# Performance work log

Measured on AMD Instinct MI355X. Metric: run time of the kernel, lower is better.

## Reference

```python
import jax, jax.numpy as jnp
import numpy as np

C = 64
RED = 4            # attention reduction: conv_match C -> C//RED
CR = C // RED      # 16, also MultiScaleSpatialAttention reduced channels
N_HASHES = 4
CHUNK = 512
RES_SCALE = 0.1
EPS = 5e-5


def conv2d(x, w, b=None, padding=0, groups=1):
    out = jax.lax.conv_general_dilated(
        x, w, (1, 1), [(padding, padding), (padding, padding)],
        dimension_numbers=('NCHW', 'OIHW', 'NCHW'), feature_group_count=groups)
    if b is not None:
        out = out + b[None, :, None, None]
    return out


def ds_conv(x, pw_w, dw_w, dw_b, padding):
    # pointwise (no bias) then depthwise (bias)
    x = conv2d(x, pw_w)
    return conv2d(x, dw_w, dw_b, padding=padding, groups=dw_w.shape[0])


def pool2(x, mode):
    B, Cc, H, W = x.shape
    xr = x.reshape(B, Cc, H // 2, 2, W // 2, 2)
    return xr.max(axis=(3, 5)) if mode == 'max' else xr.mean(axis=(3, 5))


def bilinear_ac(x, out_h, out_w):
    # bilinear interpolation with align_corners=True (matches F.interpolate)
    B, Cc, h, w = x.shape
    def coords(n_in, n_out):
        pos = jnp.arange(n_out, dtype=x.dtype) * ((n_in - 1) / (n_out - 1))
        lo = jnp.floor(pos).astype(jnp.int32)
        hi = jnp.minimum(lo + 1, n_in - 1)
        frac = pos - lo.astype(x.dtype)
        return lo, hi, frac
    lo_h, hi_h, fh = coords(h, out_h)
    x = x[:, :, lo_h, :] * (1 - fh)[None, None, :, None] + x[:, :, hi_h, :] * fh[None, None, :, None]
    lo_w, hi_w, fw = coords(w, out_w)
    x = x[:, :, :, lo_w] * (1 - fw) + x[:, :, :, hi_w] * fw
    return x


def sparse_attn(x, wm, bm, wa, ba, rot):
    # NLSN-style LSH-chunked non-local sparse attention
    N, Cc, H, W = x.shape
    L = H * W
    xe = conv2d(x, wm, bm).reshape(N, -1, L).transpose(0, 2, 1)   # [N,L,Ce]
    ye = conv2d(x, wa, ba).reshape(N, -1, L).transpose(0, 2, 1)   # [N,L,C]
    Ce = xe.shape[-1]
    n_chunks = L // CHUNK                     # L multiple of CHUNK here -> no padding
    buckets = min(n_chunks + n_chunks % 2, 128)
    # LSH hashing (rot: [Ce, n_hashes, buckets//2])
    rv = jnp.einsum('blf,fhi->bhli', xe, rot)
    rv = jnp.concatenate([rv, -rv], axis=-1)  # [N,nh,L,buckets]
    codes = jnp.argmax(rv, axis=-1) + (jnp.arange(N_HASHES) * buckets)[None, :, None]
    codes = codes.reshape(N, -1)              # [N, nh*L]
    idx = jnp.argsort(codes, axis=-1)
    undo = jnp.argsort(idx, axis=-1)
    mod_idx = idx % L
    xs = jnp.take_along_axis(xe, mod_idx[:, :, None], axis=1)     # [N,nh*L,Ce]
    ys = jnp.take_along_axis(ye, mod_idx[:, :, None], axis=1)     # [N,nh*L,C]
    xb = xs.reshape(N, N_HASHES, n_chunks, CHUNK, Ce)
    yb = ys.reshape(N, N_HASHES, n_chunks, CHUNK, Cc)
    xm = xb / jnp.maximum(jnp.linalg.norm(xb, axis=-1, keepdims=True), EPS)
    def adj(t):  # add previous / next bucket (circular)
        return jnp.concatenate([t, jnp.roll(t, 1, axis=2), jnp.roll(t, -1, axis=2)], axis=3)
    xm3, yb3 = adj(xm), adj(yb)
    raw = jnp.einsum('bhkie,bhkje->bhkij', xb, xm3)               # [N,nh,k,CHUNK,3*CHUNK]
    bscore = jax.nn.logsumexp(raw, axis=-1, keepdims=True)
    score = jnp.exp(raw - bscore)
    ret = jnp.einsum('bhkij,bhkje->bhkie', score, yb3)            # [N,nh,k,CHUNK,C]
    ret = ret.reshape(N, N_HASHES * L, Cc)
    bscore = bscore.reshape(N, N_HASHES * L)
    ret = jnp.take_along_axis(ret, undo[:, :, None], axis=1).reshape(N, N_HASHES, L, Cc)
    bscore = jnp.take_along_axis(bscore, undo, axis=1).reshape(N, N_HASHES, L, 1)
    probs = jax.nn.softmax(bscore, axis=1)                        # over hash rounds
    out = (ret * probs).sum(axis=1)                               # [N,L,C]
    out = out.transpose(0, 2, 1).reshape(N, Cc, H, W)
    return out * RES_SCALE + x


def setup_inputs() -> dict:
    key = jax.random.key(0)
    ks = iter(jax.random.split(key, 40))
    w = lambda *s: jax.random.normal(next(ks), s, jnp.float32) * 0.1
    inp = {
        'x': jax.random.normal(next(ks), (2, C, 128, 128), jnp.float32),
        'spa_down_w': w(CR, C, 1, 1), 'spa_down_b': w(CR),
        's0_pw_w': w(2 * CR, CR, 1, 1), 's0_dw_w': w(2 * CR, 1, 1, 1), 's0_dw_b': w(2 * CR),
        'br3_pw_w': w(CR, CR, 1, 1), 'br3_dw_w': w(CR, 1, 3, 3), 'br3_dw_b': w(CR),
        'br5_pw_w': w(CR, CR, 1, 1), 'br5_dw_w': w(CR, 1, 5, 5), 'br5_dw_b': w(CR),
        'br7_pw_w': w(CR, CR, 1, 1), 'br7_dw_w': w(CR, 1, 7, 7), 'br7_dw_b': w(CR),
        'fusion_w': w(C, 8 * CR, 1, 1), 'fusion_b': w(C),
        'resid_w': w(C, C, 1, 1), 'resid_b': w(C),
        'ca_w1': w(C // 16, C, 1, 1), 'ca_b1': w(C // 16),
        'ca_w2': w(C, C // 16, 1, 1), 'ca_b2': w(C),
        'conv1x1_w': w(C, C, 1, 1), 'conv1x1_b': w(C),
        'match_w': w(CR, C, 1, 1), 'match_b': w(CR),
        'asm_w': w(C, C, 1, 1), 'asm_b': w(C),
        'rot': jax.random.normal(next(ks), (CR, N_HASHES, 16), jnp.float32),  # buckets//2 = 16
        'collect_w': w(C, C, 1, 1), 'collect_b': w(C),
    }
    return inp


def reference(x, spa_down_w, spa_down_b, s0_pw_w, s0_dw_w, s0_dw_b,
              br3_pw_w, br3_dw_w, br3_dw_b, br5_pw_w, br5_dw_w, br5_dw_b,
              br7_pw_w, br7_dw_w, br7_dw_b, fusion_w, fusion_b,
              resid_w, resid_b, ca_w1, ca_b1, ca_w2, ca_b2,
              conv1x1_w, conv1x1_b, match_w, match_b, asm_w, asm_b, rot,
              collect_w, collect_b):
    B, Cc, H, W = x.shape
    # --- MultiScaleSpatialAttention ---
    xr = conv2d(x, spa_down_w, spa_down_b)                # [B,16,H,W]
    s0 = ds_conv(xr, s0_pw_w, s0_dw_w, s0_dw_b, padding=0)
    feats = [s0]
    for pw, dw, db, pad in ((br3_pw_w, br3_dw_w, br3_dw_b, 1),
                            (br5_pw_w, br5_dw_w, br5_dw_b, 2),
                            (br7_pw_w, br7_dw_w, br7_dw_b, 3)):
        mx = ds_conv(pool2(xr, 'max'), pw, dw, db, pad)
        av = ds_conv(pool2(xr, 'avg'), pw, dw, db, pad)
        feats.append(jnp.concatenate([bilinear_ac(mx, H, W), bilinear_ac(av, H, W)], axis=1))
    attn = jax.nn.sigmoid(conv2d(jnp.concatenate(feats, axis=1), fusion_w, fusion_b))
    spa_mask = x * attn + conv2d(x, resid_w, resid_b)
    # --- CALayer ---
    y = x.mean(axis=(2, 3), keepdims=True)
    y = jax.nn.sigmoid(conv2d(jax.nn.relu(conv2d(y, ca_w1, ca_b1)), ca_w2, ca_b2))
    spe_mask = x * y
    # --- combine + SparseMaskConv (n_layers=1: attention then 1x1 collect) ---
    mask = conv2d(spa_mask + spe_mask, conv1x1_w, conv1x1_b) + x
    fea = sparse_attn(mask, match_w, match_b, asm_w, asm_b, rot)
    out1 = conv2d(fea, collect_w, collect_b)
    return out1 + x
```

## Files before the change

### kernel.cpp

```cpp
#include <hip/hip_runtime.h>
#include <math.h>

static constexpr int NB = 2;
static constexpr int NC = 64;
static constexpr int NHp = 128, NWp = 128;
static constexpr int NL = NHp * NWp;
static constexpr int NCR = 16;
static constexpr int NL2 = 64 * 64;
static constexpr int NHASH = 4;
static constexpr int CHUNKSZ = 512;
static constexpr int NCHUNKS = 32;
static constexpr int TOT = NHASH * NL;
static constexpr int NKEY = 128;
static constexpr int NTILE = 256;
static constexpr int TILESZ = TOT / NTILE;

typedef _Float16 half4 __attribute__((ext_vector_type(4)));
typedef _Float16 half8 __attribute__((ext_vector_type(8)));
typedef float f32x4 __attribute__((ext_vector_type(4)));

#if __has_builtin(__builtin_amdgcn_exp2f)
  #define EXP2F(x) __builtin_amdgcn_exp2f(x)
#else
  #define EXP2F(x) __expf(0.69314718f*(x))
#endif

static constexpr size_t OFF_MASK = 0;
static constexpr size_t OFF_FEA  = OFF_MASK + (size_t)NB*NC*NL;
static constexpr size_t OFF_XE   = OFF_FEA  + (size_t)NB*NC*NL;
static constexpr size_t OFF_XEH  = OFF_XE   + (size_t)NB*NL*NCR;
static constexpr size_t OFF_XENH = OFF_XEH  + (size_t)NB*NL*NCR/2;
static constexpr size_t OFF_VS   = OFF_XENH + (size_t)NB*NL*NCR/2;
static constexpr size_t OFF_RET  = OFF_VS   + (size_t)NB*TOT*NC/2;
static constexpr size_t OFF_BSC  = OFF_RET  + (size_t)NB*TOT*NC/2;
static constexpr size_t OFF_INT  = OFF_BSC  + (size_t)NB*TOT;
static constexpr size_t IOFF_CODES = 0;
static constexpr size_t IOFF_IDX   = IOFF_CODES + (size_t)NB*TOT;
static constexpr size_t IOFF_UNDO  = IOFF_IDX   + (size_t)NB*TOT;
static constexpr size_t IOFF_HIST  = IOFF_UNDO  + (size_t)NB*TOT;
static constexpr size_t IOFF_OFFS  = IOFF_HIST  + (size_t)NB*NKEY*NTILE/2;
static constexpr size_t IOFF_END   = IOFF_OFFS  + (size_t)NB*NKEY*NTILE/2;
static constexpr size_t OFF_CAY = OFF_INT + IOFF_END;
static constexpr size_t OFF_CAS = OFF_CAY + 128;
static constexpr size_t OFF_CRW = OFF_CAS + 128;
static constexpr size_t OFF_CRB = OFF_CRW + 4096;
static constexpr size_t OFF_QS = OFF_FEA;
static constexpr size_t OFF_KS = OFF_QS + (size_t)NB*TOT*NCR/2;
static_assert(OFF_KS + (size_t)NB*TOT*NCR/2 <= OFF_XE, "qs/ks fit in fea region");
static constexpr size_t OFF_PTMP  = OFF_FEA;
static constexpr size_t OFF_DWT   = OFF_PTMP + (size_t)6*NB*NCR*NL2;
static_assert(OFF_DWT + (size_t)6*NB*NCR*NL2 <= OFF_XE, "halfres overlay fits");
static constexpr size_t OFF_XR    = OFF_XE;
static constexpr size_t OFF_FEATS = OFF_XR + (size_t)NB*NCR*NL;
static_assert(OFF_FEATS + (size_t)NB*128*NL <= OFF_RET, "feats overlay fits");
static constexpr size_t OFF_PRE1  = OFF_FEA;

__device__ __forceinline__ float sigmoidf_(float v){ return 1.0f/(1.0f + expf(-v)); }


__global__ __launch_bounds__(256,4) void k_xr(const float* __restrict__ x,
                     const float* __restrict__ w,
                     const float* __restrict__ b, float* __restrict__ xr){
  int gid = blockIdx.x*256 + threadIdx.x;
  int pix = gid >> 1, hf = gid & 1;
  int bb = pix >> 14, p = pix & (NL-1);
  const float* xi = x + (size_t)bb*NC*NL + (size_t)hf*32*NL + p;
  float acc[16];
  #pragma unroll
  for (int oc=0; oc<16; ++oc) acc[oc] = hf ? 0.f : b[oc];
  for (int ic0=0; ic0<32; ic0+=16){
    float r[16];
    #pragma unroll
    for (int j=0; j<16; ++j) r[j] = xi[(size_t)(ic0+j)*NL];
    #pragma unroll
    for (int oc=0; oc<16; ++oc){
      #pragma unroll
      for (int j=0; j<16; ++j) acc[oc] += r[j]*w[oc*64 + hf*32 + ic0 + j];
    }
  }
  #pragma unroll
  for (int oc=0; oc<16; ++oc) acc[oc] += __shfl_xor(acc[oc], 1, 64);
  if (!hf){
    float* xo = xr + (size_t)bb*NCR*NL + p;
    #pragma unroll
    for (int oc=0; oc<16; ++oc) xo[(size_t)oc*NL] = acc[oc];
  }
}

__global__ __launch_bounds__(256,4) void k_s0(const float* __restrict__ xr,
                     const float* __restrict__ pw,
                     const float* __restrict__ dww, const float* __restrict__ dwb,
                     float* __restrict__ feats){
  int gid = blockIdx.x*256 + threadIdx.x;
  int oc0 = blockIdx.y*16;
  int bb = gid >> 14, p = gid & (NL-1);
  const float* xi = xr + (size_t)bb*NCR*NL + p;
  float r[16];
  #pragma unroll
  for (int ic=0; ic<16; ++ic) r[ic] = xi[(size_t)ic*NL];
  float* fo = feats + (size_t)bb*128*NL + p;
  #pragma unroll
  for (int j=0; j<16; ++j){
    int oc = oc0 + j;
    float s = 0.f;
    #pragma unroll
    for (int ic=0; ic<16; ++ic) s += r[ic]*pw[oc*16+ic];
    fo[(size_t)oc*NL] = s*dww[oc] + dwb[oc];
  }
}

__global__ void k_pw16_all(const float* __restrict__ xr,
                           const float* __restrict__ w0, const float* __restrict__ w1,
                           const float* __restrict__ w2, float* __restrict__ out){
  int gid = blockIdx.x*256 + threadIdx.x;
  if (gid >= 6*NB*NL2) return;
  int p = gid & (NL2-1); int t = gid >> 12; int bb = t & 1; int combo = t >> 1;
  int br = combo >> 1, mode = combo & 1;
  const float* w = (br==0) ? w0 : (br==1) ? w1 : w2;
  int y = p >> 6, x2 = p & 63;
  float r[16];
  #pragma unroll
  for (int ic=0; ic<16; ++ic){
    const float* base = xr + (size_t)(bb*NCR + ic)*NL + (size_t)(2*y)*NWp + 2*x2;
    float a = base[0], b_ = base[1], c_ = base[NWp], d = base[NWp+1];
    r[ic] = mode ? 0.25f*(a+b_+c_+d) : fmaxf(fmaxf(a,b_), fmaxf(c_,d));
  }
  float* oo = out + ((size_t)(combo*NB + bb)*NCR)*NL2 + p;
  #pragma unroll
  for (int oc=0; oc<16; ++oc){
    float s = 0.f;
    #pragma unroll
    for (int ic=0; ic<16; ++ic) s += r[ic]*w[oc*16+ic];
    oo[(size_t)oc*NL2] = s;
  }
}

__global__ void k_dw_all(const float* __restrict__ in,
                         const float* __restrict__ w3, const float* __restrict__ b3,
                         const float* __restrict__ w5, const float* __restrict__ b5,
                         const float* __restrict__ w7, const float* __restrict__ b7,
                         float* __restrict__ out){
  int gid = blockIdx.x*256 + threadIdx.x;
  if (gid >= 6*NB*NCR*NL2) return;
  int p = gid & (NL2-1); int t = gid >> 12; int c = t & 15; int r2 = t >> 4;
  int bb = r2 & 1; int combo = r2 >> 1;
  int br = combo >> 1;
  int K = (br==0) ? 3 : (br==1) ? 5 : 7; int P = K >> 1;
  const float* w = (br==0) ? w3 : (br==1) ? w5 : w7;
  const float* bias = (br==0) ? b3 : (br==1) ? b5 : b7;
  int y = p >> 6, x = p & 63;
  const float* xi = in + ((size_t)(combo*NB + bb)*NCR + c)*NL2;
  float s = bias[c];
  for (int dy=0; dy<K; ++dy){
    int iy = y + dy - P;
    if ((unsigned)iy < 64u){
      for (int dx=0; dx<K; ++dx){
        int ix = x + dx - P;
        if ((unsigned)ix < 64u) s += xi[iy*64 + ix] * w[(c*K + dy)*K + dx];
      }
    }
  }
  out[gid] = s;
}

__global__ void k_up_all(const float* __restrict__ in, float* __restrict__ feats){
  int gid = blockIdx.x*256 + threadIdx.x;
  if (gid >= 6*NB*NCR*NL) return;
  int p = gid & (NL-1); int t = gid >> 14; int c = t & 15; int r2 = t >> 4;
  int bb = r2 & 1; int combo = r2 >> 1;
  int y = p >> 7, x = p & 127;
  const float sc = 63.0f/127.0f;
  float fy = y*sc; int ly = (int)floorf(fy); int hy = min(ly+1, 63); fy -= (float)ly;
  float fx = x*sc; int lx = (int)floorf(fx); int hx = min(lx+1, 63); float gx = fx - (float)lx;
  const float* xi = in + ((size_t)(combo*NB + bb)*NCR + c)*NL2;
  float v0 = xi[ly*64+lx]*(1.f-fy) + xi[hy*64+lx]*fy;
  float v1 = xi[ly*64+hx]*(1.f-fy) + xi[hy*64+hx]*fy;
  int coff = 32 + combo*16 + c;
  feats[(size_t)bb*128*NL + (size_t)coff*NL + p] = v0*(1.f-gx) + v1*gx;
}

__global__ void k_camean(const float* __restrict__ x, float* __restrict__ cay){
  __shared__ float red[256];
  int bc = blockIdx.x; int tid = threadIdx.x;
  float s = 0.f;
  for (int i = tid; i < NL; i += 256) s += x[(size_t)bc*NL + i];
  red[tid] = s; __syncthreads();
  for (int st=128; st>0; st>>=1){ if (tid<st) red[tid]+=red[tid+st]; __syncthreads(); }
  if (tid==0) cay[bc] = red[0] / (float)NL;
}

__global__ void k_camlp(const float* __restrict__ cay,
                        const float* __restrict__ w1, const float* __restrict__ b1,
                        const float* __restrict__ w2, const float* __restrict__ b2,
                        float* __restrict__ cas){
  __shared__ float z[NB*4];
  int tid = threadIdx.x;
  if (tid < NB*4){
    int bb = tid >> 2, j = tid & 3;
    float s = b1[j];
    for (int ic=0; ic<NC; ++ic) s += cay[bb*NC+ic]*w1[j*NC+ic];
    z[tid] = fmaxf(s, 0.f);
  }
  __syncthreads();
  if (tid < NB*NC){
    int bb = tid >> 6, oc = tid & 63;
    float s = b2[oc];
    #pragma unroll
    for (int j=0; j<4; ++j) s += z[bb*4+j]*w2[oc*4+j];
    cas[tid] = sigmoidf_(s);
  }
}

__global__ void k_wprod(const float* __restrict__ c11w, const float* __restrict__ c11b,
                        const float* __restrict__ rw, const float* __restrict__ rb,
                        float* __restrict__ crw, float* __restrict__ crb){
  int gid = blockIdx.x*256 + threadIdx.x;
  if (gid >= 4096) return;
  int o = gid >> 6, i = gid & 63;
  float s = 0.f;
  for (int k=0; k<64; ++k) s += c11w[o*64+k]*rw[k*64+i];
  crw[gid] = s;
  if (i == 0){
    float t = c11b[o];
    for (int k=0; k<64; ++k) t += c11w[o*64+k]*rb[k];
    crb[o] = t;
  }
}

__global__ __launch_bounds__(256,4) void k_attnmul(const float* __restrict__ x,
                          const float* __restrict__ feats,
                          const float* __restrict__ fw, const float* __restrict__ fb,
                          const float* __restrict__ cas, float* __restrict__ pre1){
  int gid = blockIdx.x*256 + threadIdx.x;
  int oc0 = blockIdx.y*16;
  int bb = gid >> 14, p = gid & (NL-1);
  const float* fi = feats + (size_t)bb*128*NL + p;
  float acc[16];
  #pragma unroll
  for (int j=0; j<16; ++j) acc[j] = fb[oc0+j];
  for (int k0=0; k0<128; k0+=8){
    float fr[8];
    #pragma unroll
    for (int j=0; j<8; ++j) fr[j] = fi[(size_t)(k0+j)*NL];
    #pragma unroll
    for (int j=0; j<16; ++j){
      #pragma unroll
      for (int t=0; t<8; ++t) acc[j] += fr[t]*fw[(oc0+j)*128+k0+t];
    }
  }
  const float* xb = x + (size_t)bb*NC*NL + p;
  float* po = pre1 + (size_t)bb*NC*NL + p;
  #pragma unroll
  for (int j=0; j<16; ++j){
    int oc = oc0 + j;
    float xv = xb[(size_t)oc*NL];
    po[(size_t)oc*NL] = xv*(sigmoidf_(acc[j]) + cas[bb*64+oc]);
  }
}

__global__ __launch_bounds__(256,4) void k_mask(const float* __restrict__ pre1,
                       const float* __restrict__ c11w,
                       const float* __restrict__ crw, const float* __restrict__ crb,
                       const float* __restrict__ x, float* __restrict__ mask){
  int gid = blockIdx.x*256 + threadIdx.x;
  int oc0 = blockIdx.y*16;
  int bb = gid >> 14, p = gid & (NL-1);
  const float* pi = pre1 + (size_t)bb*NC*NL + p;
  const float* xi = x + (size_t)bb*NC*NL + p;
  float acc[16];
  #pragma unroll
  for (int j=0; j<16; ++j) acc[j] = crb[oc0+j];
  for (int ic0=0; ic0<64; ic0+=8){
    float pr[8], xr8[8];
    #pragma unroll
    for (int j=0; j<8; ++j){ pr[j] = pi[(size_t)(ic0+j)*NL]; xr8[j] = xi[(size_t)(ic0+j)*NL]; }
    #pragma unroll
    for (int j=0; j<16; ++j){
      #pragma unroll
      for (int t=0; t<8; ++t)
        acc[j] += pr[t]*c11w[(oc0+j)*64+ic0+t] + xr8[t]*crw[(oc0+j)*64+ic0+t];
    }
  }
  float* mo = mask + (size_t)bb*NC*NL + p;
  #pragma unroll
  for (int j=0; j<16; ++j){
    int oc = oc0 + j;
    mo[(size_t)oc*NL] = acc[j] + xi[(size_t)oc*NL];
  }
}


__global__ __launch_bounds__(256,4) void k_xe(const float* __restrict__ mask,
                     const float* __restrict__ w, const float* __restrict__ b,
                     const float* __restrict__ rot,
                     _Float16* __restrict__ xeh, _Float16* __restrict__ xenh,
                     int* __restrict__ codes, int* __restrict__ hist){
  int gid = blockIdx.x*256 + threadIdx.x;
  int pix = gid >> 1, hf = gid & 1;
  int bb = pix >> 14, l = pix & (NL-1);
  const float* mi = mask + (size_t)bb*NC*NL + (size_t)hf*32*NL + l;
  float acc[16];
  #pragma unroll
  for (int oc=0; oc<16; ++oc) acc[oc] = hf ? 0.f : b[oc];
  for (int ic0=0; ic0<32; ic0+=16){
    float r[16];
    #pragma unroll
    for (int j=0; j<16; ++j) r[j] = mi[(size_t)(ic0+j)*NL];
    #pragma unroll
    for (int oc=0; oc<16; ++oc){
      #pragma unroll
      for (int j=0; j<16; ++j) acc[oc] += r[j]*w[oc*64 + hf*32 + ic0 + j];
    }
  }
  #pragma unroll
  for (int oc=0; oc<16; ++oc) acc[oc] += __shfl_xor(acc[oc], 1, 64);
  if (!hf){
    float n2 = 0.f;
    #pragma unroll
    for (int oc=0; oc<16; ++oc) n2 += acc[oc]*acc[oc];
    float inv = 1.0f / fmaxf(sqrtf(n2), 5e-5f);
    _Float16* ho = xeh + (size_t)pix*NCR;
    _Float16* no = xenh + (size_t)pix*NCR;
    #pragma unroll
    for (int g=0; g<4; ++g){
      half4 hv, nv;
      #pragma unroll
      for (int j=0; j<4; ++j){ hv[j] = (_Float16)acc[g*4+j]; nv[j] = (_Float16)(acc[g*4+j]*inv); }
      *(half4*)(ho + g*4) = hv;
      *(half4*)(no + g*4) = nv;
    }
  }
  #pragma unroll
  for (int hh=0; hh<2; ++hh){
    int h = hf*2 + hh;
    float rv[16];
    #pragma unroll
    for (int i=0; i<16; ++i){
      float s = 0.f;
      #pragma unroll
      for (int f=0; f<16; ++f) s += acc[f]*rot[(f*NHASH + h)*16 + i];
      rv[i] = s;
    }
    float best = -1e30f; int bi = 0;
    #pragma unroll
    for (int i=0; i<16; ++i){ if (rv[i] > best){ best = rv[i]; bi = i; } }
    #pragma unroll
    for (int i=0; i<16; ++i){ float val = -rv[i]; if (val > best){ best = val; bi = 16+i; } }
    int code = bi + h*32;
    codes[((bb*NHASH + h) << 14) + l] = code;
    int tile = h*64 + (l >> 8);
    atomicAdd(&hist[bb*NKEY*NTILE + code*NTILE + tile], 1);
  }
}

__global__ __launch_bounds__(256,4) void k_yeh(const float* __restrict__ mask,
                      const float* __restrict__ w, const float* __restrict__ b,
                      const int* __restrict__ undo, _Float16* __restrict__ vs){
  int gid = blockIdx.x*256 + threadIdx.x;
  int oc0 = blockIdx.y*16;
  int bb = gid >> 14, l = gid & (NL-1);
  const float* mi = mask + (size_t)bb*NC*NL + l;
  float acc[16];
  #pragma unroll
  for (int j=0; j<16; ++j) acc[j] = b[oc0+j];
  for (int ic0=0; ic0<64; ic0+=8){
    float r[8];
    #pragma unroll
    for (int j=0; j<8; ++j) r[j] = mi[(size_t)(ic0+j)*NL];
    #pragma unroll
    for (int j=0; j<16; ++j){
      #pragma unroll
      for (int t=0; t<8; ++t) acc[j] += r[t]*w[(oc0+j)*64+ic0+t];
    }
  }
  half8 h0, h1;
  #pragma unroll
  for (int j=0; j<8; ++j){ h0[j] = (_Float16)acc[j]; h1[j] = (_Float16)acc[8+j]; }
  const int* ub = undo + bb*TOT;
  #pragma unroll
  for (int h=0; h<4; ++h){
    int pos = ub[h*NL + l];
    _Float16* vo = vs + ((size_t)bb*TOT + pos)*64 + oc0;
    *(half8*)(vo) = h0;
    *(half8*)(vo + 8) = h1;
  }
}

__global__ void k_scan(const int* __restrict__ hist, int* __restrict__ offs){
  __shared__ int part[256];
  int bb = blockIdx.x; int t = threadIdx.x;
  const int* hi = hist + (size_t)bb*NKEY*NTILE;
  int* oo = offs + (size_t)bb*NKEY*NTILE;
  int s = 0;
  for (int i=0; i<128; ++i) s += hi[t*128 + i];
  part[t] = s; __syncthreads();
  int v = s;
  for (int off=1; off<256; off<<=1){
    int u = (t >= off) ? part[t-off] : 0;
    __syncthreads();
    v += u; part[t] = v;
    __syncthreads();
  }
  int run = v - s;
  for (int i=0; i<128; ++i){ int q = hi[t*128+i]; oo[t*128+i] = run; run += q; }
}

__global__ __launch_bounds__(256) void k_scatter(const int* __restrict__ codes,
                          const int* __restrict__ offs,
                          const _Float16* __restrict__ xeh, const _Float16* __restrict__ xenh,
                          int* __restrict__ idx, int* __restrict__ undo,
                          _Float16* __restrict__ qs, _Float16* __restrict__ ks){
  __shared__ int cnt[4][NKEY];
  int wid = threadIdx.x >> 6, lane = threadIdx.x & 63;
  int t4 = blockIdx.x;
  int bb = t4 >> 6;
  int tile = (t4 & 63)*4 + wid;
  cnt[wid][lane] = 0; cnt[wid][64+lane] = 0;
  const int* cb = codes + bb*TOT;
  const int* ob = offs + (size_t)bb*NKEY*NTILE;
  int* ib = idx + bb*TOT;
  int* ub = undo + bb*TOT;
  for (int g=0; g<4; ++g){
    int j = tile*TILESZ + g*64 + lane;
    int k = cb[j];
    unsigned long long m = ~0ull;
    #pragma unroll
    for (int bit=0; bit<7; ++bit){
      unsigned long long bmask = __ballot((k >> bit) & 1);
      m &= ((k >> bit) & 1) ? bmask : ~bmask;
    }
    int rank = __popcll(m & ((1ull << lane) - 1ull));
    int leader = __ffsll((unsigned long long)m) - 1;
    int base = 0;
    if (lane == leader){
      base = cnt[wid][k];
      cnt[wid][k] = base + __popcll(m);
    }
    base = __shfl(base, leader, 64);
    int pos = ob[k*NTILE + tile] + base + rank;
    ib[pos] = j;
    ub[j] = pos;
    int l = j & (NL-1);
    const _Float16* qp = xeh + ((size_t)bb*NL + l)*16;
    const _Float16* kp = xenh + ((size_t)bb*NL + l)*16;
    _Float16* qo = qs + ((size_t)bb*TOT + pos)*16;
    _Float16* ko = ks + ((size_t)bb*TOT + pos)*16;
    *(half8*)(qo)     = *(const half8*)(qp);
    *(half8*)(qo + 8) = *(const half8*)(qp + 8);
    *(half8*)(ko)     = *(const half8*)(kp);
    *(half8*)(ko + 8) = *(const half8*)(kp + 8);
    __threadfence_block();
  }
}

__global__ __launch_bounds__(512) void k_attn(
    const _Float16* __restrict__ qs, const _Float16* __restrict__ ks,
    const _Float16* __restrict__ vs,
    _Float16* __restrict__ retb, float* __restrict__ bsc){
  __shared__ _Float16 kt[64*20];
  __shared__ _Float16 vt[64*70];
  int blk = blockIdx.x;
  int qh = blk & 1; int kk = (blk >> 1) & 31; int h = (blk >> 6) & 3; int bb = blk >> 8;
  int tid = threadIdx.x;
  int w = tid >> 6, lane = tid & 63, col = lane & 15, grp = lane >> 4;
  int qbase = h*NL + kk*CHUNKSZ + qh*256 + w*32;

  half4 qfr[2]; int posq[2];
  #pragma unroll
  for (int qf=0; qf<2; ++qf){
    posq[qf] = qbase + qf*16 + col;
    qfr[qf] = *(const half4*)(qs + ((size_t)bb*TOT + posq[qf])*16 + grp*4);
    #pragma unroll
    for (int i=0; i<4; ++i) qfr[qf][i] = (_Float16)((float)qfr[qf][i] * 1.44269504f);
  }

  f32x4 O[4][2];
  #pragma unroll
  for (int a=0; a<4; ++a)
    #pragma unroll
    for (int b=0; b<2; ++b) O[a][b] = (f32x4){0.f,0.f,0.f,0.f};
  float m_[2] = {-1e30f,-1e30f};
  float ssum[2] = {0.f,0.f};

  int kx = tid & 63, c0 = (tid >> 6) * 8;
  int kr = tid >> 1, khf = tid & 1;

  #define SPOS(jj) ({ int sec_ = (jj) >> 9; int j0_ = (jj) & 511; \
      int cc_ = kk + ((sec_==1) ? -1 : (sec_==2) ? 1 : 0); \
      cc_ = (cc_ + NCHUNKS) & (NCHUNKS-1); h*NL + cc_*CHUNKSZ + j0_; })

  half8 vv = *(const half8*)(vs + ((size_t)bb*TOT + SPOS(kx))*64 + c0);
  half8 kv;
  if (tid < 128) kv = *(const half8*)(ks + ((size_t)bb*TOT + SPOS(kr))*16 + khf*8);

  for (int t=0; t<24; ++t){
    __syncthreads();
    #pragma unroll
    for (int j=0; j<8; ++j) vt[(c0+j)*70 + kx] = vv[j];
    if (tid < 128) *(half8*)(kt + kr*20 + khf*8) = kv;
    __syncthreads();
    if (t+1 < 24){
      int jj = (t+1)*64;
      vv = *(const half8*)(vs + ((size_t)bb*TOT + SPOS(jj + kx))*64 + c0);
      if (tid < 128) kv = *(const half8*)(ks + ((size_t)bb*TOT + SPOS(jj + kr))*16 + khf*8);
    }

    f32x4 S[4][2];
    #pragma unroll
    for (int kb=0; kb<4; ++kb){
      half4 ka = *(const half4*)(kt + (kb*16 + col)*20 + grp*4);
      #pragma unroll
      for (int qf=0; qf<2; ++qf)
        S[kb][qf] = __builtin_amdgcn_mfma_f32_16x16x16f16(
            ka, qfr[qf], (f32x4){0.f,0.f,0.f,0.f}, 0, 0, 0);
    }

    half8 pb[2][2];
    #pragma unroll
    for (int qf=0; qf<2; ++qf){
      float mtl = -1e30f;
      #pragma unroll
      for (int kb=0; kb<4; ++kb)
        #pragma unroll
        for (int i=0; i<4; ++i) mtl = fmaxf(mtl, S[kb][qf][i]);
      if (__any(mtl > m_[qf] + 11.5f)){
        float mt = fmaxf(mtl, __shfl_xor(mtl, 16, 64));
        mt = fmaxf(mt, __shfl_xor(mt, 32, 64));
        float mn = fmaxf(m_[qf], mt);
        float sc = EXP2F(m_[qf] - mn);
        ssum[qf] *= sc;
        m_[qf] = mn;
        #pragma unroll
        for (int cf=0; cf<4; ++cf)
          #pragma unroll
          for (int i=0; i<4; ++i) O[cf][qf][i] *= sc;
      }
      float ps = 0.f;
      #pragma unroll
      for (int k2=0; k2<2; ++k2){
        half8 hb;
        #pragma unroll
        for (int i=0; i<4; ++i){
          float p0 = EXP2F(S[2*k2][qf][i]   - m_[qf]);
          float p1 = EXP2F(S[2*k2+1][qf][i] - m_[qf]);
          ps += p0 + p1;
          hb[i]   = (_Float16)p0;
          hb[4+i] = (_Float16)p1;
        }
        pb[qf][k2] = hb;
      }
      ssum[qf] += ps;
    }

    #pragma unroll
    for (int cf=0; cf<4; ++cf){
      #pragma unroll
      for (int k2=0; k2<2; ++k2){
        half4 a0 = *(const half4*)(vt + (cf*16 + col)*70 + k2*32 + grp*4);
        half4 a1 = *(const half4*)(vt + (cf*16 + col)*70 + k2*32 + 16 + grp*4);
        half8 va;
        #pragma unroll
        for (int i=0; i<4; ++i){ va[i] = a0[i]; va[4+i] = a1[i]; }
        #pragma unroll
        for (int qf=0; qf<2; ++qf)
          O[cf][qf] = __builtin_amdgcn_mfma_f32_16x16x32_f16(
              va, pb[qf][k2], O[cf][qf], 0, 0, 0);
      }
    }
  }
  #undef SPOS

  #pragma unroll
  for (int qf=0; qf<2; ++qf){
    float st = ssum[qf];
    st += __shfl_xor(st, 16, 64);
    st += __shfl_xor(st, 32, 64);
    float inv = 1.0f/st;
    size_t rb = ((size_t)bb*TOT + posq[qf])*64;
    #pragma unroll
    for (int cf=0; cf<4; ++cf){
      half4 o;
      #pragma unroll
      for (int i=0; i<4; ++i) o[i] = (_Float16)(O[cf][qf][i]*inv);
      *(half4*)(retb + rb + cf*16 + grp*4) = o;
    }
    if (grp == 0) bsc[(size_t)bb*TOT + posq[qf]] = m_[qf]*0.69314718f + logf(st);
  }
}

__global__ __launch_bounds__(256,4) void k_combine(const _Float16* __restrict__ retb,
                          const float* __restrict__ bsc,
                          const int* __restrict__ undo, const float* __restrict__ mask,
                          float* __restrict__ fea){
  int gid = blockIdx.x*256 + threadIdx.x;
  int c0 = blockIdx.y*32;
  int bb = gid >> 14; int l = gid & (NL-1);
  const int* ub = undo + bb*TOT;
  int pos[4]; float sc[4];
  #pragma unroll
  for (int h=0; h<4; ++h){ pos[h] = ub[h*NL + l]; sc[h] = bsc[bb*TOT + pos[h]]; }
  float mx = fmaxf(fmaxf(sc[0],sc[1]), fmaxf(sc[2],sc[3]));
  float e[4]; float tot = 0.f;
  #pragma unroll
  for (int h=0; h<4; ++h){ e[h] = __expf(sc[h]-mx); tot += e[h]; }
  float inv = 0.1f/tot;
  const float* mb_ = mask + (size_t)bb*NC*NL + l;
  float* fo = fea + (size_t)bb*NC*NL + l;
  const _Float16* r0 = retb + ((size_t)bb*TOT + pos[0])*NC + c0;
  const _Float16* r1 = retb + ((size_t)bb*TOT + pos[1])*NC + c0;
  const _Float16* r2 = retb + ((size_t)bb*TOT + pos[2])*NC + c0;
  const _Float16* r3 = retb + ((size_t)bb*TOT + pos[3])*NC + c0;
  #pragma unroll
  for (int g=0; g<4; ++g){
    half8 v0 = *(const half8*)(r0 + g*8);
    half8 v1 = *(const half8*)(r1 + g*8);
    half8 v2 = *(const half8*)(r2 + g*8);
    half8 v3 = *(const half8*)(r3 + g*8);
    #pragma unroll
    for (int j=0; j<8; ++j){
      int c = c0 + g*8 + j;
      float v = (float)v0[j]*e[0] + (float)v1[j]*e[1] + (float)v2[j]*e[2] + (float)v3[j]*e[3];
      fo[(size_t)c*NL] = v*inv + mb_[(size_t)c*NL];
    }
  }
}

__global__ __launch_bounds__(256,4) void k_collect(const float* __restrict__ fea,
                          const float* __restrict__ w,
                          const float* __restrict__ b, const float* __restrict__ x,
                          float* __restrict__ out){
  int gid = blockIdx.x*256 + threadIdx.x;
  int oc0 = blockIdx.y*16;
  int bb = gid >> 14, p = gid & (NL-1);
  const float* fi = fea + (size_t)bb*NC*NL + p;
  const float* xi = x + (size_t)bb*NC*NL + p;
  float acc[16];
  #pragma unroll
  for (int j=0; j<16; ++j) acc[j] = b[oc0+j];
  for (int ic0=0; ic0<64; ic0+=8){
    float r[8];
    #pragma unroll
    for (int j=0; j<8; ++j) r[j] = fi[(size_t)(ic0+j)*NL];
    #pragma unroll
    for (int j=0; j<16; ++j){
      #pragma unroll
      for (int t=0; t<8; ++t) acc[j] += r[t]*w[(oc0+j)*64+ic0+t];
    }
  }
  float* oo = out + (size_t)bb*NC*NL + p;
  #pragma unroll
  for (int j=0; j<16; ++j){
    int oc = oc0 + j;
    oo[(size_t)oc*NL] = acc[j] + xi[(size_t)oc*NL];
  }
}

extern "C" void kernel_launch(void* const* d_in, const int* in_sizes, int n_in,
                              void* d_out, int out_size, void* d_ws, size_t ws_size,
                              hipStream_t stream) {
  const float* x        = (const float*)d_in[0];
  const float* spa_dw   = (const float*)d_in[1];
  const float* spa_db   = (const float*)d_in[2];
  const float* s0_pw    = (const float*)d_in[3];
  const float* s0_dww   = (const float*)d_in[4];
  const float* s0_dwb   = (const float*)d_in[5];
  const float* fus_w    = (const float*)d_in[15];
  const float* fus_b    = (const float*)d_in[16];
  const float* res_w    = (const float*)d_in[17];
  const float* res_b    = (const float*)d_in[18];
  const float* ca_w1    = (const float*)d_in[19];
  const float* ca_b1    = (const float*)d_in[20];
  const float* ca_w2    = (const float*)d_in[21];
  const float* ca_b2    = (const float*)d_in[22];
  const float* c11_w    = (const float*)d_in[23];
  const float* c11_b    = (const float*)d_in[24];
  const float* match_w  = (const float*)d_in[25];
  const float* match_b  = (const float*)d_in[26];
  const float* asm_w    = (const float*)d_in[27];
  const float* asm_b    = (const float*)d_in[28];
  const float* rot      = (const float*)d_in[29];
  const float* col_w    = (const float*)d_in[30];
  const float* col_b    = (const float*)d_in[31];
  float* out = (float*)d_out;

  float* ws    = (float*)d_ws;
  float* mask  = ws + OFF_MASK;
  float* fea   = ws + OFF_FEA;
  _Float16* xeh  = (_Float16*)(ws + OFF_XEH);
  _Float16* xenh = (_Float16*)(ws + OFF_XENH);
  _Float16* vsort = (_Float16*)(ws + OFF_VS);
  _Float16* qsort = (_Float16*)(ws + OFF_QS);
  _Float16* ksort = (_Float16*)(ws + OFF_KS);
  _Float16* retb = (_Float16*)(ws + OFF_RET);
  float* bsc   = ws + OFF_BSC;
  int*   ib    = (int*)(ws + OFF_INT);
  int* codes   = ib + IOFF_CODES;
  int* idx     = ib + IOFF_IDX;
  int* undo    = ib + IOFF_UNDO;
  int* hist    = ib + IOFF_HIST;
  int* offs    = ib + IOFF_OFFS;
  float* cay   = ws + OFF_CAY;
  float* cas   = ws + OFF_CAS;
  float* crw   = ws + OFF_CRW;
  float* crb   = ws + OFF_CRB;
  float* xr    = ws + OFF_XR;
  float* feats = ws + OFF_FEATS;
  float* ptmp  = ws + OFF_PTMP;
  float* dwt   = ws + OFF_DWT;
  float* pre1  = ws + OFF_PRE1;

  k_xr<<<(NB*NL*2)/256, 256, 0, stream>>>(x, spa_dw, spa_db, xr);
  k_wprod<<<16, 256, 0, stream>>>(c11_w, c11_b, res_w, res_b, crw, crb);
  k_s0<<<dim3((NB*NL)/256, 2), 256, 0, stream>>>(xr, s0_pw, s0_dww, s0_dwb, feats);
  k_pw16_all<<<(6*NB*NL2)/256, 256, 0, stream>>>(xr,
      (const float*)d_in[6], (const float*)d_in[9], (const float*)d_in[12], ptmp);
  k_dw_all<<<(6*NB*NCR*NL2)/256, 256, 0, stream>>>(ptmp,
      (const float*)d_in[7], (const float*)d_in[8],
      (const float*)d_in[10], (const float*)d_in[11],
      (const float*)d_in[13], (const float*)d_in[14], dwt);
  k_up_all<<<(6*NB*NCR*NL)/256, 256, 0, stream>>>(dwt, feats);
  k_camean<<<NB*NC, 256, 0, stream>>>(x, cay);
  k_camlp<<<1, 128, 0, stream>>>(cay, ca_w1, ca_b1, ca_w2, ca_b2, cas);
  k_attnmul<<<dim3((NB*NL)/256, 4), 256, 0, stream>>>(x, feats, fus_w, fus_b, cas, pre1);
  k_mask<<<dim3((NB*NL)/256, 4), 256, 0, stream>>>(pre1, c11_w, crw, crb, x, mask);

  (void)hipMemsetAsync(hist, 0, (size_t)NB*NKEY*NTILE*sizeof(int), stream);
  k_xe<<<(NB*NL*2)/256, 256, 0, stream>>>(mask, match_w, match_b, rot, xeh, xenh, codes, hist);
  k_scan<<<NB, 256, 0, stream>>>(hist, offs);
  k_scatter<<<NB*NTILE/4, 256, 0, stream>>>(codes, offs, xeh, xenh, idx, undo, qsort, ksort);
  k_yeh<<<dim3((NB*NL)/256, 4), 256, 0, stream>>>(mask, asm_w, asm_b, undo, vsort);
  k_attn<<<NB*NHASH*NCHUNKS*2, 512, 0, stream>>>(qsort, ksort, vsort, retb, bsc);
  k_combine<<<dim3((NB*NL)/256, 2), 256, 0, stream>>>(retb, bsc, undo, mask, fea);
  k_collect<<<dim3((NB*NL)/256, 4), 256, 0, stream>>>(fea, col_w, col_b, x, out);
}
```

Baseline: 317.1 us.

## Stage pixel tiles in shared memory for 1x1 conv kernels and merge combine channels

The pointwise-conv kernels (attnmul, mask, yeh, collect) now load a 64-pixel by all-input-channel tile into LDS once per block. The 512 threads then each compute 8 output channels from that tile. Previously the input was re-read from global memory by 4 separate blockIdx.y groups. k_combine now handles all 64 channels per thread instead of splitting channels over two grid rows, so the undo/score gather runs once. The cost is lower parallelism per kernel (fewer, larger blocks), plus LDS use and a barrier.

```diff
diff --git a/kernel.cpp b/kernel.cpp
--- a/kernel.cpp
+++ b/kernel.cpp
@@ -227,65 +227,81 @@
   }
 }
 
-__global__ __launch_bounds__(256,4) void k_attnmul(const float* __restrict__ x,
+__global__ __launch_bounds__(512) void k_attnmul(const float* __restrict__ x,
                           const float* __restrict__ feats,
                           const float* __restrict__ fw, const float* __restrict__ fb,
                           const float* __restrict__ cas, float* __restrict__ pre1){
-  int gid = blockIdx.x*256 + threadIdx.x;
-  int oc0 = blockIdx.y*16;
-  int bb = gid >> 14, p = gid & (NL-1);
-  const float* fi = feats + (size_t)bb*128*NL + p;
-  float acc[16];
-  #pragma unroll
-  for (int j=0; j<16; ++j) acc[j] = fb[oc0+j];
+  __shared__ float fs[128][64];
+  int blk = blockIdx.x;
+  int bb = blk >> 8; int px0 = (blk & 255)*64;
+  int tid = threadIdx.x;
+  const float* fbase = feats + (size_t)bb*128*NL + px0;
+  for (int i = tid; i < 128*64; i += 512){
+    int k = i >> 6, p = i & 63;
+    fs[k][p] = fbase[(size_t)k*NL + p];
+  }
+  __syncthreads();
+  int px = tid & 63, oc0 = (tid >> 6)*8;
+  float acc[8];
+  #pragma unroll
+  for (int j=0; j<8; ++j) acc[j] = fb[oc0+j];
   for (int k0=0; k0<128; k0+=8){
     float fr[8];
     #pragma unroll
-    for (int j=0; j<8; ++j) fr[j] = fi[(size_t)(k0+j)*NL];
-    #pragma unroll
-    for (int j=0; j<16; ++j){
+    for (int t=0; t<8; ++t) fr[t] = fs[k0+t][px];
+    #pragma unroll
+    for (int j=0; j<8; ++j){
       #pragma unroll
       for (int t=0; t<8; ++t) acc[j] += fr[t]*fw[(oc0+j)*128+k0+t];
     }
   }
-  const float* xb = x + (size_t)bb*NC*NL + p;
-  float* po = pre1 + (size_t)bb*NC*NL + p;
-  #pragma unroll
-  for (int j=0; j<16; ++j){
+  const float* xb = x + (size_t)bb*NC*NL + px0 + px;
+  float* po = pre1 + (size_t)bb*NC*NL + px0 + px;
+  #pragma unroll
+  for (int j=0; j<8; ++j){
     int oc = oc0 + j;
     float xv = xb[(size_t)oc*NL];
     po[(size_t)oc*NL] = xv*(sigmoidf_(acc[j]) + cas[bb*64+oc]);
   }
 }
 
-__global__ __launch_bounds__(256,4) void k_mask(const float* __restrict__ pre1,
+__global__ __launch_bounds__(512) void k_mask(const float* __restrict__ pre1,
                        const float* __restrict__ c11w,
                        const float* __restrict__ crw, const float* __restrict__ crb,
                        const float* __restrict__ x, float* __restrict__ mask){
-  int gid = blockIdx.x*256 + threadIdx.x;
-  int oc0 = blockIdx.y*16;
-  int bb = gid >> 14, p = gid & (NL-1);
-  const float* pi = pre1 + (size_t)bb*NC*NL + p;
-  const float* xi = x + (size_t)bb*NC*NL + p;
-  float acc[16];
-  #pragma unroll
-  for (int j=0; j<16; ++j) acc[j] = crb[oc0+j];
+  __shared__ float ps[64][64];
+  __shared__ float xs[64][64];
+  int blk = blockIdx.x;
+  int bb = blk >> 8; int px0 = (blk & 255)*64;
+  int tid = threadIdx.x;
+  const float* pbase = pre1 + (size_t)bb*NC*NL + px0;
+  const float* xbase = x + (size_t)bb*NC*NL + px0;
+  for (int i = tid; i < 64*64; i += 512){
+    int c = i >> 6, p = i & 63;
+    ps[c][p] = pbase[(size_t)c*NL + p];
+    xs[c][p] = xbase[(size_t)c*NL + p];
+  }
+  __syncthreads();
+  int px = tid & 63, oc0 = (tid >> 6)*8;
+  float acc[8];
+  #pragma unroll
+  for (int j=0; j<8; ++j) acc[j] = crb[oc0+j];
   for (int ic0=0; ic0<64; ic0+=8){
     float pr[8], xr8[8];
     #pragma unroll
-    for (int j=0; j<8; ++j){ pr[j] = pi[(size_t)(ic0+j)*NL]; xr8[j] = xi[(size_t)(ic0+j)*NL]; }
-    #pragma unroll
-    for (int j=0; j<16; ++j){
+    for (int t=0; t<8; ++t){ pr[t] = ps[ic0+t][px]; xr8[t] = xs[ic0+t][px]; }
+    #pragma unroll
+    for (int j=0; j<8; ++j){
       #pragma unroll
       for (int t=0; t<8; ++t)
         acc[j] += pr[t]*c11w[(oc0+j)*64+ic0+t] + xr8[t]*crw[(oc0+j)*64+ic0+t];
     }
   }
-  float* mo = mask + (size_t)bb*NC*NL + p;
-  #pragma unroll
-  for (int j=0; j<16; ++j){
+  float* mo = mask + (size_t)bb*NC*NL + px0 + px;
+  #pragma unroll
+  for (int j=0; j<8; ++j){
     int oc = oc0 + j;
-    mo[(size_t)oc*NL] = acc[j] + xi[(size_t)oc*NL];
+    mo[(size_t)oc*NL] = acc[j] + xs[oc][px];
   }
 }
 
@@ -353,36 +369,42 @@
   }
 }
 
-__global__ __launch_bounds__(256,4) void k_yeh(const float* __restrict__ mask,
+__global__ __launch_bounds__(512) void k_yeh(const float* __restrict__ mask,
                       const float* __restrict__ w, const float* __restrict__ b,
                       const int* __restrict__ undo, _Float16* __restrict__ vs){
-  int gid = blockIdx.x*256 + threadIdx.x;
-  int oc0 = blockIdx.y*16;
-  int bb = gid >> 14, l = gid & (NL-1);
-  const float* mi = mask + (size_t)bb*NC*NL + l;
-  float acc[16];
-  #pragma unroll
-  for (int j=0; j<16; ++j) acc[j] = b[oc0+j];
+  __shared__ float ms[64][64];
+  int blk = blockIdx.x;
+  int bb = blk >> 8; int px0 = (blk & 255)*64;
+  int tid = threadIdx.x;
+  const float* mbase = mask + (size_t)bb*NC*NL + px0;
+  for (int i = tid; i < 64*64; i += 512){
+    int c = i >> 6, p = i & 63;
+    ms[c][p] = mbase[(size_t)c*NL + p];
+  }
+  __syncthreads();
+  int px = tid & 63, oc0 = (tid >> 6)*8;
+  float acc[8];
+  #pragma unroll
+  for (int j=0; j<8; ++j) acc[j] = b[oc0+j];
   for (int ic0=0; ic0<64; ic0+=8){
     float r[8];
     #pragma unroll
-    for (int j=0; j<8; ++j) r[j] = mi[(size_t)(ic0+j)*NL];
-    #pragma unroll
-    for (int j=0; j<16; ++j){
+    for (int t=0; t<8; ++t) r[t] = ms[ic0+t][px];
+    #pragma unroll
+    for (int j=0; j<8; ++j){
       #pragma unroll
       for (int t=0; t<8; ++t) acc[j] += r[t]*w[(oc0+j)*64+ic0+t];
     }
   }
-  half8 h0, h1;
-  #pragma unroll
-  for (int j=0; j<8; ++j){ h0[j] = (_Float16)acc[j]; h1[j] = (_Float16)acc[8+j]; }
+  half8 hv;
+  #pragma unroll
+  for (int j=0; j<8; ++j) hv[j] = (_Float16)acc[j];
+  int l = px0 + px;
   const int* ub = undo + bb*TOT;
   #pragma unroll
   for (int h=0; h<4; ++h){
     int pos = ub[h*NL + l];
-    _Float16* vo = vs + ((size_t)bb*TOT + pos)*64 + oc0;
-    *(half8*)(vo) = h0;
-    *(half8*)(vo + 8) = h1;
+    *(half8*)(vs + ((size_t)bb*TOT + pos)*64 + oc0) = hv;
   }
 }
 
@@ -593,7 +615,6 @@
                           const int* __restrict__ undo, const float* __restrict__ mask,
                           float* __restrict__ fea){
   int gid = blockIdx.x*256 + threadIdx.x;
-  int c0 = blockIdx.y*32;
   int bb = gid >> 14; int l = gid & (NL-1);
   const int* ub = undo + bb*TOT;
   int pos[4]; float sc[4];
@@ -606,50 +627,56 @@
   float inv = 0.1f/tot;
   const float* mb_ = mask + (size_t)bb*NC*NL + l;
   float* fo = fea + (size_t)bb*NC*NL + l;
-  const _Float16* r0 = retb + ((size_t)bb*TOT + pos[0])*NC + c0;
-  const _Float16* r1 = retb + ((size_t)bb*TOT + pos[1])*NC + c0;
-  const _Float16* r2 = retb + ((size_t)bb*TOT + pos[2])*NC + c0;
-  const _Float16* r3 = retb + ((size_t)bb*TOT + pos[3])*NC + c0;
-  #pragma unroll
-  for (int g=0; g<4; ++g){
+  const _Float16* r0 = retb + ((size_t)bb*TOT + pos[0])*NC;
+  const _Float16* r1 = retb + ((size_t)bb*TOT + pos[1])*NC;
+  const _Float16* r2 = retb + ((size_t)bb*TOT + pos[2])*NC;
+  const _Float16* r3 = retb + ((size_t)bb*TOT + pos[3])*NC;
+  for (int g=0; g<8; ++g){
     half8 v0 = *(const half8*)(r0 + g*8);
     half8 v1 = *(const half8*)(r1 + g*8);
     half8 v2 = *(const half8*)(r2 + g*8);
     half8 v3 = *(const half8*)(r3 + g*8);
     #pragma unroll
     for (int j=0; j<8; ++j){
-      int c = c0 + g*8 + j;
+      int c = g*8 + j;
       float v = (float)v0[j]*e[0] + (float)v1[j]*e[1] + (float)v2[j]*e[2] + (float)v3[j]*e[3];
       fo[(size_t)c*NL] = v*inv + mb_[(size_t)c*NL];
     }
   }
 }
 
-__global__ __launch_bounds__(256,4) void k_collect(const float* __restrict__ fea,
+__global__ __launch_bounds__(512) void k_collect(const float* __restrict__ fea,
                           const float* __restrict__ w,
                           const float* __restrict__ b, const float* __restrict__ x,
                           float* __restrict__ out){
-  int gid = blockIdx.x*256 + threadIdx.x;
-  int oc0 = blockIdx.y*16;
-  int bb = gid >> 14, p = gid & (NL-1);
-  const float* fi = fea + (size_t)bb*NC*NL + p;
-  const float* xi = x + (size_t)bb*NC*NL + p;
-  float acc[16];
-  #pragma unroll
-  for (int j=0; j<16; ++j) acc[j] = b[oc0+j];
+  __shared__ float fs[64][64];
+  int blk = blockIdx.x;
+  int bb = blk >> 8; int px0 = (blk & 255)*64;
+  int tid = threadIdx.x;
+  const float* fbase = fea + (size_t)bb*NC*NL + px0;
+  for (int i = tid; i < 64*64; i += 512){
+    int c = i >> 6, p = i & 63;
+    fs[c][p] = fbase[(size_t)c*NL + p];
+  }
+  __syncthreads();
+  int px = tid & 63, oc0 = (tid >> 6)*8;
+  float acc[8];
+  #pragma unroll
+  for (int j=0; j<8; ++j) acc[j] = b[oc0+j];
   for (int ic0=0; ic0<64; ic0+=8){
     float r[8];
     #pragma unroll
-    for (int j=0; j<8; ++j) r[j] = fi[(size_t)(ic0+j)*NL];
-    #pragma unroll
-    for (int j=0; j<16; ++j){
+    for (int t=0; t<8; ++t) r[t] = fs[ic0+t][px];
+    #pragma unroll
+    for (int j=0; j<8; ++j){
       #pragma unroll
       for (int t=0; t<8; ++t) acc[j] += r[t]*w[(oc0+j)*64+ic0+t];
     }
   }
-  float* oo = out + (size_t)bb*NC*NL + p;
-  #pragma unroll
-  for (int j=0; j<16; ++j){
+  const float* xi = x + (size_t)bb*NC*NL + px0 + px;
+  float* oo = out + (size_t)bb*NC*NL + px0 + px;
+  #pragma unroll
+  for (int j=0; j<8; ++j){
     int oc = oc0 + j;
     oo[(size_t)oc*NL] = acc[j] + xi[(size_t)oc*NL];
   }
@@ -721,15 +748,15 @@
   k_up_all<<<(6*NB*NCR*NL)/256, 256, 0, stream>>>(dwt, feats);
   k_camean<<<NB*NC, 256, 0, stream>>>(x, cay);
   k_camlp<<<1, 128, 0, stream>>>(cay, ca_w1, ca_b1, ca_w2, ca_b2, cas);
-  k_attnmul<<<dim3((NB*NL)/256, 4), 256, 0, stream>>>(x, feats, fus_w, fus_b, cas, pre1);
-  k_mask<<<dim3((NB*NL)/256, 4), 256, 0, stream>>>(pre1, c11_w, crw, crb, x, mask);
+  k_attnmul<<<NB*NL/64, 512, 0, stream>>>(x, feats, fus_w, fus_b, cas, pre1);
+  k_mask<<<NB*NL/64, 512, 0, stream>>>(pre1, c11_w, crw, crb, x, mask);
 
   (void)hipMemsetAsync(hist, 0, (size_t)NB*NKEY*NTILE*sizeof(int), stream);
   k_xe<<<(NB*NL*2)/256, 256, 0, stream>>>(mask, match_w, match_b, rot, xeh, xenh, codes, hist);
   k_scan<<<NB, 256, 0, stream>>>(hist, offs);
   k_scatter<<<NB*NTILE/4, 256, 0, stream>>>(codes, offs, xeh, xenh, idx, undo, qsort, ksort);
-  k_yeh<<<dim3((NB*NL)/256, 4), 256, 0, stream>>>(mask, asm_w, asm_b, undo, vsort);
+  k_yeh<<<NB*NL/64, 512, 0, stream>>>(mask, asm_w, asm_b, undo, vsort);
   k_attn<<<NB*NHASH*NCHUNKS*2, 512, 0, stream>>>(qsort, ksort, vsort, retb, bsc);
-  k_combine<<<dim3((NB*NL)/256, 2), 256, 0, stream>>>(retb, bsc, undo, mask, fea);
-  k_collect<<<dim3((NB*NL)/256, 4), 256, 0, stream>>>(fea, col_w, col_b, x, out);
-}
+  k_combine<<<(NB*NL)/256, 256, 0, stream>>>(retb, bsc, undo, mask, fea);
+  k_collect<<<NB*NL/64, 512, 0, stream>>>(fea, col_w, col_b, x, out);
+}
```

New measurement: 341.0 us. 7.5% more time.
